# Performance work log

Measured on AMD Instinct MI355X. Metric: run time of the kernel, lower is better.

Reference implementation:

```python
import jax, jax.numpy as jnp
import numpy as np

VOCAB = 32002        # len(tokenizer) + 2
N_HIDDEN = 512
N_COND = 1024
MAX_LENGTH = 15
BATCH = 256


def setup_inputs() -> dict:
    key = jax.random.key(0)
    ks = jax.random.split(key, 12)
    s = 0.02
    return {
        "caption": jax.random.randint(ks[0], (BATCH, 1), 0, VOCAB, dtype=jnp.int64) if jax.config.jax_enable_x64 else jax.random.randint(ks[0], (BATCH, 1), 0, VOCAB, dtype=jnp.int32),
        "img": jax.random.normal(ks[1], (BATCH, N_COND), dtype=jnp.float32),
        "embedding": jax.random.normal(ks[2], (VOCAB, N_HIDDEN), dtype=jnp.float32) * s,
        "W_cond": jax.random.normal(ks[3], (N_HIDDEN, N_COND), dtype=jnp.float32) * s,
        "b_cond": jnp.zeros((N_HIDDEN,), dtype=jnp.float32),
        "w_ih": jax.random.normal(ks[4], (3 * N_HIDDEN, N_HIDDEN), dtype=jnp.float32) * s,
        "w_hh": jax.random.normal(ks[5], (3 * N_HIDDEN, N_HIDDEN), dtype=jnp.float32) * s,
        "b_ih": jnp.zeros((3 * N_HIDDEN,), dtype=jnp.float32),
        "b_hh": jnp.zeros((3 * N_HIDDEN,), dtype=jnp.float32),
        "W_pred": jax.random.normal(ks[6], (VOCAB, N_HIDDEN), dtype=jnp.float32) * s,
        "b_pred": jnp.zeros((VOCAB,), dtype=jnp.float32),
    }


def gru_cell(x, h, w_ih, w_hh, b_ih, b_hh):
    # PyTorch GRUCell math: gates ordered (reset, update, new)
    gi = x @ w_ih.T + b_ih   # [B, 3H]
    gh = h @ w_hh.T + b_hh   # [B, 3H]
    i_r, i_z, i_n = jnp.split(gi, 3, axis=-1)
    h_r, h_z, h_n = jnp.split(gh, 3, axis=-1)
    r = jax.nn.sigmoid(i_r + h_r)
    z = jax.nn.sigmoid(i_z + h_z)
    n = jnp.tanh(i_n + r * h_n)
    return (1.0 - z) * n + z * h


def reference(caption, img, embedding, W_cond, b_cond, w_ih, w_hh, b_ih, b_hh, W_pred, b_pred):
    h0 = img @ W_cond.T + b_cond           # [B, H] initial GRU hidden state
    tok0 = caption[:, 0].astype(jnp.int32)  # seed token

    def step(carry, _):
        h, tok = carry
        x = embedding[tok]                              # [B, H] gather
        h_new = gru_cell(x, h, w_ih, w_hh, b_ih, b_hh)  # [B, H]
        logits = h_new @ W_pred.T + b_pred              # [B, V]
        nxt = jnp.argmax(logits, axis=-1).astype(jnp.int32)  # top-1 == topk(1)
        return (h_new, nxt), nxt

    (_, _), toks = jax.lax.scan(step, (h0, tok0), None, length=MAX_LENGTH - 1)
    # toks: [T-1, B] -> predictions [B, T] with seed token in column 0
    preds = jnp.concatenate([tok0[:, None], toks.T], axis=1)
    return preds
```

## Files before the change

### kernel.cpp

```cpp
#include <hip/hip_runtime.h>
#include <math.h>

#define BATCH 256
#define NH 512
#define NCOND 1024
#define NV 32002
#define NT 15
#define NVT_F32 501
#define NVT_MF  251

#define SP_P  4096256
#define SP_IH 196608
#define SP_HH 196608
#define SP_C  131072
#define SPLIT_W_BLOCKS 16001
#define SPLIT_S_BLOCKS 2048

typedef short short8 __attribute__((ext_vector_type(8)));
typedef float float4v __attribute__((ext_vector_type(4)));

__device__ __forceinline__ void async_load16(const void* g, void* l){
  __builtin_amdgcn_global_load_lds(
      (const __attribute__((address_space(1))) void*)g,
      (__attribute__((address_space(3))) void*)l, 16, 0, 0);
}

__device__ __forceinline__ void split2(float x, unsigned short& hi, unsigned short& lo){
  unsigned u = __float_as_uint(x);
  unsigned r = u + 0x7fffu + ((u >> 16) & 1u);
  hi = (unsigned short)(r >> 16);
  float fh = __uint_as_float(r & 0xffff0000u);
  float res = x - fh;
  unsigned u2 = __float_as_uint(res);
  unsigned r2 = u2 + 0x7fffu + ((u2 >> 16) & 1u);
  lo = (unsigned short)(r2 >> 16);
}

__device__ __forceinline__ unsigned long long pack_key(float v, int idx){
  unsigned u = __float_as_uint(v);
  u = (u & 0x80000000u) ? ~u : (u | 0x80000000u);
  return ((unsigned long long)u << 32) | (unsigned)(0x7fffffff - idx);
}
__device__ __forceinline__ int key_tok(unsigned long long k){
  return 0x7fffffff - (int)(unsigned)(k & 0xffffffffu);
}

__global__ void k_seed(const int* __restrict__ cap, int* __restrict__ preds){
  int b = threadIdx.x;
  preds[b*NT + 0] = cap[b];
}

__global__ __launch_bounds__(256) void k_split_w(const float* __restrict__ Wp,
    unsigned short* __restrict__ Whi, unsigned short* __restrict__ Wlo){
  size_t i = (size_t)blockIdx.x * 256 + threadIdx.x;
  float4 v = *(const float4*)(Wp + i*4);
  unsigned short h0,l0,h1,l1,h2,l2,h3,l3;
  split2(v.x,h0,l0); split2(v.y,h1,l1); split2(v.z,h2,l2); split2(v.w,h3,l3);
  ushort4 hs = {h0,h1,h2,h3};
  ushort4 ls = {l0,l1,l2,l3};
  *(ushort4*)(Whi + i*4) = hs;
  *(ushort4*)(Wlo + i*4) = ls;
}

__global__ __launch_bounds__(256) void k_split_small(
    const float* __restrict__ wih, const float* __restrict__ whh,
    const float* __restrict__ Wc,
    unsigned short* __restrict__ W6hi, unsigned short* __restrict__ W6lo,
    unsigned short* __restrict__ Wchi, unsigned short* __restrict__ Wclo){
  size_t i = (size_t)blockIdx.x * 256 + threadIdx.x;
  const float* src; unsigned short *dh, *dl; size_t off;
  if (i < SP_IH){ src = wih; dh = W6hi; dl = W6lo; off = i; }
  else if (i < SP_IH + SP_HH){
    src = whh; dh = W6hi + 786432; dl = W6lo + 786432; off = i - SP_IH;
  } else { src = Wc; dh = Wchi; dl = Wclo; off = i - SP_IH - SP_HH; }
  float4 v = *(const float4*)(src + off*4);
  unsigned short h0,l0,h1,l1,h2,l2,h3,l3;
  split2(v.x,h0,l0); split2(v.y,h1,l1); split2(v.z,h2,l2); split2(v.w,h3,l3);
  ushort4 hs = {h0,h1,h2,h3};
  ushort4 ls = {l0,l1,l2,l3};
  *(ushort4*)(dh + off*4) = hs;
  *(ushort4*)(dl + off*4) = ls;
}

__global__ __launch_bounds__(256) void k_h0_mf(
    const float* __restrict__ img,
    const unsigned short* __restrict__ Wchi, const unsigned short* __restrict__ Wclo,
    const float* __restrict__ bc,
    float* __restrict__ h0,
    unsigned short* __restrict__ hhi, unsigned short* __restrict__ hlo){
  __shared__ __align__(16) unsigned short sA[2][16*64];
  __shared__ __align__(16) unsigned short sB[2][64*64];
  int tid = threadIdx.x, w = tid >> 6, lane = tid & 63;
  int jbase = blockIdx.x * 16, bbase = blockIdx.y * 64;
  int r16 = lane & 15, q = lane >> 4;
  float4v acc = {0.f,0.f,0.f,0.f};
  for (int k0 = 0; k0 < NCOND; k0 += 64){
    {
      int arr = w >> 1, t = w & 1;
      int a = t*8 + (lane >> 3);
      int p = (lane & 7) ^ (lane >> 3);
      const unsigned short* gs = (arr ? Wclo : Wchi) + (size_t)(jbase + a)*NCOND + k0 + p*8;
      async_load16(gs, (char*)&sA[arr][0] + t*1024);
    }
    #pragma unroll
    for (int i = 0; i < 2; i++){
      int u = tid + 256*i;
      int b = u >> 3, s = u & 7;
      int p = s ^ (b & 7);
      const float* gp = img + (size_t)(bbase + b)*NCOND + k0 + p*8;
      float4 f0 = *(const float4*)gp, f1 = *(const float4*)(gp + 4);
      short8 hv, lv; unsigned short hh, ll;
      split2(f0.x,hh,ll); hv[0]=(short)hh; lv[0]=(short)ll;
      split2(f0.y,hh,ll); hv[1]=(short)hh; lv[1]=(short)ll;
      split2(f0.z,hh,ll); hv[2]=(short)hh; lv[2]=(short)ll;
      split2(f0.w,hh,ll); hv[3]=(short)hh; lv[3]=(short)ll;
      split2(f1.x,hh,ll); hv[4]=(short)hh; lv[4]=(short)ll;
      split2(f1.y,hh,ll); hv[5]=(short)hh; lv[5]=(short)ll;
      split2(f1.z,hh,ll); hv[6]=(short)hh; lv[6]=(short)ll;
      split2(f1.w,hh,ll); hv[7]=(short)hh; lv[7]=(short)ll;
      *(short8*)((char*)&sB[0][0] + b*128 + s*16) = hv;
      *(short8*)((char*)&sB[1][0] + b*128 + s*16) = lv;
    }
    __syncthreads();
    int rb = w*16 + r16;
    #pragma unroll
    for (int kh = 0; kh < 2; kh++){
      int pa = kh*4 + q;
      int offA = r16*128 + ((pa ^ (r16 & 7))*16);
      int offB = rb*128 + ((pa ^ (rb & 7))*16);
      short8 ah = *(const short8*)((const char*)&sA[0][0] + offA);
      short8 al = *(const short8*)((const char*)&sA[1][0] + offA);
      short8 bh = *(const short8*)((const char*)&sB[0][0] + offB);
      short8 bl = *(const short8*)((const char*)&sB[1][0] + offB);
      acc = __builtin_amdgcn_mfma_f32_16x16x32_bf16(ah, bh, acc, 0,0,0);
      acc = __builtin_amdgcn_mfma_f32_16x16x32_bf16(ah, bl, acc, 0,0,0);
      acc = __builtin_amdgcn_mfma_f32_16x16x32_bf16(al, bh, acc, 0,0,0);
    }
    __syncthreads();
  }
  int b = bbase + w*16 + r16;
  #pragma unroll
  for (int reg = 0; reg < 4; reg++){
    int j = jbase + q*4 + reg;
    float val = acc[reg] + bc[j];
    h0[(size_t)b*NH + j] = val;
    unsigned short sh, sl; split2(val, sh, sl);
    hhi[(size_t)b*NH + j] = sh;
    hlo[(size_t)b*NH + j] = sl;
  }
}

__global__ __launch_bounds__(256) void k_gru_mf(
    const int* __restrict__ cap,
    const unsigned long long* __restrict__ slot_prev,
    const float* __restrict__ emb,
    const unsigned short* __restrict__ W6hi, const unsigned short* __restrict__ W6lo,
    const unsigned short* __restrict__ Hhi, const unsigned short* __restrict__ Hlo,
    const float* __restrict__ bih, const float* __restrict__ bhh,
    const float* __restrict__ hprev, float* __restrict__ hnew,
    unsigned short* __restrict__ nhhi, unsigned short* __restrict__ nhlo,
    int* __restrict__ preds, int use_caption, int pred_col){
  __shared__ __align__(16) unsigned short sAh[96*128];
  __shared__ __align__(16) unsigned short sAl[96*128];
  __shared__ __align__(16) unsigned short sXh[32*128];
  __shared__ __align__(16) unsigned short sXl[32*128];
  __shared__ __align__(16) unsigned short sHh[32*128];
  __shared__ __align__(16) unsigned short sHl[32*128];
  __shared__ float comb[2][768];
  __shared__ int tok[32];
  int tid = threadIdx.x, w = tid >> 6, lane = tid & 63;
  int jbase = blockIdx.x * 16, bbase = blockIdx.y * 32;
  int bsub = w & 1, grp = w >> 1;
  int b16 = lane & 15, q = lane >> 4;

  if (tid < 32){
    int t;
    if (use_caption) t = cap[bbase + tid];
    else {
      t = key_tok(slot_prev[bbase + tid]);
      if (blockIdx.x == 0) preds[(bbase + tid)*NT + pred_col] = t;
    }
    tok[tid] = t;
  }
  __syncthreads();
  int tr0 = tok[tid >> 4];
  int tr1 = tok[16 + (tid >> 4)];

  float4v acc[3];
  #pragma unroll
  for (int g = 0; g < 3; g++) acc[g] = (float4v){0.f,0.f,0.f,0.f};

  for (int k0 = 0; k0 < NH; k0 += 128){
    #pragma unroll
    for (int i = 0; i < 12; i++){
      int idx = w*12 + i;
      int arr = idx >= 24, t = arr ? (idx - 24) : idx;
      int row = t*4 + (lane >> 4);
      int glocal = row >> 4, jr = row & 15;
      int slot = (lane & 15) ^ (row & 15);
      const unsigned short* gs = (arr ? W6lo : W6hi)
          + (size_t)(glocal*512 + jbase + jr)*NH + k0 + slot*8;
      async_load16(gs, (char*)(arr ? sAl : sAh) + t*1024);
    }
    #pragma unroll
    for (int i = 0; i < 4; i++){
      int idx = w*4 + i;
      int arr = idx >= 8, t = idx & 7;
      int row = t*4 + (lane >> 4);
      int slot = (lane & 15) ^ (row & 15);
      const unsigned short* gs = (arr ? Hlo : Hhi)
          + (size_t)(bbase + row)*NH + k0 + slot*8;
      async_load16(gs, (char*)(arr ? sHl : sHh) + t*1024);
    }
    #pragma unroll
    for (int i = 0; i < 2; i++){
      int u = tid + 256*i;
      int row = u >> 4, slot = u & 15;
      int phys = slot ^ (row & 15);
      int tr = i ? tr1 : tr0;
      const float* gp = emb + (size_t)tr*NH + k0 + slot*8;
      float4 f0 = *(const float4*)gp, f1 = *(const float4*)(gp + 4);
      short8 hv, lv; unsigned short hh, ll;
      split2(f0.x,hh,ll); hv[0]=(short)hh; lv[0]=(short)ll;
      split2(f0.y,hh,ll); hv[1]=(short)hh; lv[1]=(short)ll;
      split2(f0.z,hh,ll); hv[2]=(short)hh; lv[2]=(short)ll;
      split2(f0.w,hh,ll); hv[3]=(short)hh; lv[3]=(short)ll;
      split2(f1.x,hh,ll); hv[4]=(short)hh; lv[4]=(short)ll;
      split2(f1.y,hh,ll); hv[5]=(short)hh; lv[5]=(short)ll;
      split2(f1.z,hh,ll); hv[6]=(short)hh; lv[6]=(short)ll;
      split2(f1.w,hh,ll); hv[7]=(short)hh; lv[7]=(short)ll;
      *(short8*)((char*)sXh + row*256 + phys*16) = hv;
      *(short8*)((char*)sXl + row*256 + phys*16) = lv;
    }
    __syncthreads();
    #pragma unroll
    for (int kh = 0; kh < 4; kh++){
      int phys = (kh*4 + q) ^ b16;
      int boff = (bsub*16 + b16)*256 + phys*16;
      short8 bh = grp ? *(const short8*)((const char*)sHh + boff)
                      : *(const short8*)((const char*)sXh + boff);
      short8 bl = grp ? *(const short8*)((const char*)sHl + boff)
                      : *(const short8*)((const char*)sXl + boff);
      #pragma unroll
      for (int gi = 0; gi < 3; gi++){
        int row = (grp*3 + gi)*16 + b16;
        int aoff = row*256 + phys*16;
        short8 ah = *(const short8*)((const char*)sAh + aoff);
        short8 al = *(const short8*)((const char*)sAl + aoff);
        acc[gi] = __builtin_amdgcn_mfma_f32_16x16x32_bf16(ah, bh, acc[gi], 0,0,0);
        acc[gi] = __builtin_amdgcn_mfma_f32_16x16x32_bf16(ah, bl, acc[gi], 0,0,0);
        acc[gi] = __builtin_amdgcn_mfma_f32_16x16x32_bf16(al, bh, acc[gi], 0,0,0);
      }
    }
    __syncthreads();
  }

  if (grp == 1){
    #pragma unroll
    for (int gi = 0; gi < 3; gi++)
      #pragma unroll
      for (int reg = 0; reg < 4; reg++)
        comb[bsub][gi*256 + b16*16 + q*4 + reg] = acc[gi][reg];
  }
  __syncthreads();
  if (grp == 0){
    int b = bbase + bsub*16 + b16;
    #pragma unroll
    for (int reg = 0; reg < 4; reg++){
      int jl = q*4 + reg;
      int j = jbase + jl;
      float hr = comb[bsub][0*256 + b16*16 + jl];
      float hz = comb[bsub][1*256 + b16*16 + jl];
      float hn = comb[bsub][2*256 + b16*16 + jl];
      float gr = acc[0][reg] + hr + bih[j] + bhh[j];
      float gz = acc[1][reg] + hz + bih[j+NH] + bhh[j+NH];
      float in_ = acc[2][reg] + bih[j+2*NH];
      float hn_ = hn + bhh[j+2*NH];
      float r = 1.f/(1.f + expf(-gr));
      float z = 1.f/(1.f + expf(-gz));
      float n = tanhf(in_ + r*hn_);
      float hp = hprev[(size_t)b*NH + j];
      float val = (1.f - z)*n + z*hp;
      hnew[(size_t)b*NH + j] = val;
      unsigned short sh, sl; split2(val, sh, sl);
      nhhi[(size_t)b*NH + j] = sh;
      nhlo[(size_t)b*NH + j] = sl;
    }
  }
}

__global__ __launch_bounds__(256) void k_pred_mf(
    const unsigned short* __restrict__ Hhi, const unsigned short* __restrict__ Hlo,
    const unsigned short* __restrict__ Whi, const unsigned short* __restrict__ Wlo,
    const float* __restrict__ bp,
    unsigned long long* __restrict__ slot){
  __shared__ __align__(16) unsigned short sAh[128*64];
  __shared__ __align__(16) unsigned short sAl[128*64];
  __shared__ __align__(16) unsigned short sBh[128*64];
  __shared__ __align__(16) unsigned short sBl[128*64];
  __shared__ float sval[256];
  __shared__ int   sidx[256];
  int tid = threadIdx.x, w = tid >> 6, lane = tid & 63;
  int vt = blockIdx.x, vbase = vt*128, bbase = blockIdx.y*128;
  int mhalf = w & 1, nhalf = w >> 1;
  unsigned short* mybuf = (w==0)?sAh:(w==1)?sAl:(w==2)?sBh:sBl;
  const unsigned short* gsrc = (w==0)?Whi:(w==1)?Wlo:(w==2)?Hhi:Hlo;
  int rowbase = (w < 2) ? vbase : bbase;
  int isA = (w < 2);
  int rl = lane >> 3, sl = lane & 7;
  int pq = sl ^ rl;
  float4v acc[4][4];
  #pragma unroll
  for (int mi=0;mi<4;mi++)
    #pragma unroll
    for (int ni=0;ni<4;ni++) acc[mi][ni] = (float4v){0.f,0.f,0.f,0.f};
  int q = lane >> 4, b16 = lane & 15;

  for (int k0 = 0; k0 < NH; k0 += 64){
    #pragma unroll
    for (int t = 0; t < 16; t++){
      int grow = rowbase + t*8 + rl;
      if (isA && grow > NV-1) grow = NV-1;
      const unsigned short* gp = gsrc + (size_t)grow*NH + k0 + pq*8;
      async_load16(gp, (char*)mybuf + t*1024);
    }
    __syncthreads();
    #pragma unroll
    for (int kh = 0; kh < 2; kh++){
      int pa = kh*4 + q;
      short8 ah[4], al[4], bh[4], bl[4];
      #pragma unroll
      for (int mi=0;mi<4;mi++){
        int r = mhalf*64 + mi*16 + b16;
        int off = r*128 + ((pa ^ (r & 7))*16);
        ah[mi] = *(const short8*)((const char*)sAh + off);
        al[mi] = *(const short8*)((const char*)sAl + off);
      }
      #pragma unroll
      for (int ni=0;ni<4;ni++){
        int r = nhalf*64 + ni*16 + b16;
        int off = r*128 + ((pa ^ (r & 7))*16);
        bh[ni] = *(const short8*)((const char*)sBh + off);
        bl[ni] = *(const short8*)((const char*)sBl + off);
      }
      #pragma unroll
      for (int mi=0;mi<4;mi++)
        #pragma unroll
        for (int ni=0;ni<4;ni++){
          acc[mi][ni] = __builtin_amdgcn_mfma_f32_16x16x32_bf16(ah[mi], bh[ni], acc[mi][ni], 0,0,0);
          acc[mi][ni] = __builtin_amdgcn_mfma_f32_16x16x32_bf16(ah[mi], bl[ni], acc[mi][ni], 0,0,0);
          acc[mi][ni] = __builtin_amdgcn_mfma_f32_16x16x32_bf16(al[mi], bh[ni], acc[mi][ni], 0,0,0);
        }
    }
    __syncthreads();
  }

  float bestv[4] = {-INFINITY,-INFINITY,-INFINITY,-INFINITY};
  int   besti[4] = {0x7fffffff,0x7fffffff,0x7fffffff,0x7fffffff};
  #pragma unroll
  for (int mi=0;mi<4;mi++){
    #pragma unroll
    for (int reg=0;reg<4;reg++){
      int v = vbase + mhalf*64 + mi*16 + q*4 + reg;
      if (v < NV){
        float bpv = bp[v];
        #pragma unroll
        for (int ni=0;ni<4;ni++){
          float cand = acc[mi][ni][reg] + bpv;
          if (cand > bestv[ni] || (cand == bestv[ni] && v < besti[ni])){
            bestv[ni] = cand; besti[ni] = v;
          }
        }
      }
    }
  }
  #pragma unroll
  for (int ni=0;ni<4;ni++){
    #pragma unroll
    for (int off=16; off<=32; off<<=1){
      float ov = __shfl_xor(bestv[ni], off);
      int   oi = __shfl_xor(besti[ni], off);
      if (ov > bestv[ni] || (ov == bestv[ni] && oi < besti[ni])){
        bestv[ni] = ov; besti[ni] = oi;
      }
    }
    if (lane < 16){
      sval[w*64 + ni*16 + b16] = bestv[ni];
      sidx[w*64 + ni*16 + b16] = besti[ni];
    }
  }
  __syncthreads();
  if (tid < 128){
    int nh = tid >> 6;
    int wA = nh*2, wB = nh*2 + 1;
    int slotid = tid & 63;
    float vA = sval[wA*64 + slotid], vB = sval[wB*64 + slotid];
    int   iA = sidx[wA*64 + slotid], iB = sidx[wB*64 + slotid];
    bool takeB = (vB > vA) || (vB == vA && iB < iA);
    float bv = takeB ? vB : vA;
    int   bi = takeB ? iB : iA;
    atomicMax(slot + bbase + tid, pack_key(bv, bi));
  }
}

__global__ void k_fin_slot(const unsigned long long* __restrict__ slot,
                           int* __restrict__ preds){
  int b = threadIdx.x;
  preds[b*NT + (NT-1)] = key_tok(slot[b]);
}

__global__ __launch_bounds__(256) void k_h0_fb(const float* __restrict__ img,
                                            const float* __restrict__ Wc,
                                            const float* __restrict__ bc,
                                            float* __restrict__ h0){
  __shared__ float As[64*36];
  __shared__ float Bs[64*36];
  int tid = threadIdx.x;
  int tx = tid & 15, ty = tid >> 4;
  int jbase = blockIdx.x * 64;
  int bbase = blockIdx.y * 64;
  int lrow = tid >> 3;
  int lc4  = (tid & 7) << 2;
  float acc[4][4] = {};
  for (int k0 = 0; k0 < NCOND; k0 += 32){
    #pragma unroll
    for (int rr = 0; rr < 64; rr += 32){
      *(float4*)&As[(lrow+rr)*36 + lc4] =
          *(const float4*)(img + (size_t)(bbase+lrow+rr)*NCOND + k0 + lc4);
      *(float4*)&Bs[(lrow+rr)*36 + lc4] =
          *(const float4*)(Wc + (size_t)(jbase+lrow+rr)*NCOND + k0 + lc4);
    }
    __syncthreads();
    #pragma unroll
    for (int kk = 0; kk < 32; kk += 4){
      float4 a[4], w[4];
      #pragma unroll
      for (int i=0;i<4;i++) a[i] = *(float4*)&As[(ty+16*i)*36+kk];
      #pragma unroll
      for (int j=0;j<4;j++) w[j] = *(float4*)&Bs[(tx+16*j)*36+kk];
      #pragma unroll
      for (int i=0;i<4;i++)
        #pragma unroll
        for (int j=0;j<4;j++)
          acc[i][j] += a[i].x*w[j].x + a[i].y*w[j].y + a[i].z*w[j].z + a[i].w*w[j].w;
    }
    __syncthreads();
  }
  #pragma unroll
  for (int i=0;i<4;i++){
    int b = bbase + ty + 16*i;
    #pragma unroll
    for (int j=0;j<4;j++){
      int jj = jbase + tx + 16*j;
      h0[(size_t)b*NH + jj] = acc[i][j] + bc[jj];
    }
  }
}

__global__ __launch_bounds__(256) void k_pred_f32(const float* __restrict__ h,
                                              const float* __restrict__ Wp,
                                              const float* __restrict__ bp,
                                              float* __restrict__ pval,
                                              int* __restrict__ pidx){
  __shared__ float As[64*36];
  __shared__ float Bs[64*36];
  __shared__ float rv[64*16];
  __shared__ int   ri[64*16];
  int tid = threadIdx.x;
  int tx = tid & 15, ty = tid >> 4;
  int vt = blockIdx.x;
  int vbase = vt * 64;
  int bbase = blockIdx.y * 64;
  int lrow = tid >> 3;
  int lc4  = (tid & 7) << 2;
  float acc[4][4] = {};
  for (int k0 = 0; k0 < NH; k0 += 32){
    #pragma unroll
    for (int rr = 0; rr < 64; rr += 32){
      *(float4*)&As[(lrow+rr)*36 + lc4] =
          *(const float4*)(h + (size_t)(bbase+lrow+rr)*NH + k0 + lc4);
      int v = vbase + lrow + rr;
      float4 wv = make_float4(0.f,0.f,0.f,0.f);
      if (v < NV) wv = *(const float4*)(Wp + (size_t)v*NH + k0 + lc4);
      *(float4*)&Bs[(lrow+rr)*36 + lc4] = wv;
    }
    __syncthreads();
    #pragma unroll
    for (int kk = 0; kk < 32; kk += 4){
      float4 a[4], wv[4];
      #pragma unroll
      for (int i=0;i<4;i++) a[i] = *(float4*)&As[(ty+16*i)*36+kk];
      #pragma unroll
      for (int j=0;j<4;j++) wv[j] = *(float4*)&Bs[(tx+16*j)*36+kk];
      #pragma unroll
      for (int i=0;i<4;i++)
        #pragma unroll
        for (int j=0;j<4;j++)
          acc[i][j] += a[i].x*wv[j].x + a[i].y*wv[j].y + a[i].z*wv[j].z + a[i].w*wv[j].w;
    }
    __syncthreads();
  }
  #pragma unroll
  for (int i=0;i<4;i++){
    int bl = ty + 16*i;
    float best = -INFINITY; int bidx = 0;
    #pragma unroll
    for (int j=0;j<4;j++){
      int v = vbase + tx + 16*j;
      if (v < NV){
        float val = acc[i][j] + bp[v];
        if (val > best){ best = val; bidx = v; }
      }
    }
    rv[bl*16+tx] = best; ri[bl*16+tx] = bidx;
  }
  __syncthreads();
  if (tid < 64){
    float best = -INFINITY; int bidx = 0;
    #pragma unroll
    for (int t=0;t<16;t++){
      float v = rv[tid*16+t];
      if (v > best){ best = v; bidx = ri[tid*16+t]; }
    }
    pval[vt*BATCH + bbase + tid] = best;
    pidx[vt*BATCH + bbase + tid] = bidx;
  }
}

__global__ __launch_bounds__(256) void k_gru_fb(const int* __restrict__ cap,
    const float* __restrict__ pval, const int* __restrict__ pidx,
    const float* __restrict__ emb,
    const float* __restrict__ wih, const float* __restrict__ whh,
    const float* __restrict__ bih, const float* __restrict__ bhh,
    const float* __restrict__ hprev, float* __restrict__ hnew,
    int* __restrict__ preds, int use_caption, int pred_col, int nvt){
  __shared__ int   s_tok[32];
  __shared__ float rav[32*8];
  __shared__ int   rai[32*8];
  __shared__ float xs[32*36];
  __shared__ float hs[32*36];
  __shared__ float wis[3*16*36];
  __shared__ float whs[3*16*36];
  int tid = threadIdx.x;
  int tx = tid & 15, ty = tid >> 4;
  int jbase = blockIdx.x * 16;
  int bbase = blockIdx.y * 32;

  if (use_caption){
    if (tid < 32) s_tok[tid] = cap[bbase + tid];
  } else {
    int bl = tid >> 3, l8 = tid & 7;
    float best = -INFINITY; int bidx = 0x7fffffff;
    for (int p = l8; p < nvt; p += 8){
      float v = pval[p*BATCH + bbase + bl];
      int   i = pidx[p*BATCH + bbase + bl];
      if (v > best || (v == best && i < bidx)){ best = v; bidx = i; }
    }
    rav[bl*8 + l8] = best; rai[bl*8 + l8] = bidx;
    __syncthreads();
    if (tid < 32){
      float bb = -INFINITY; int bi = 0x7fffffff;
      #pragma unroll
      for (int t=0;t<8;t++){
        float v = rav[tid*8+t]; int i = rai[tid*8+t];
        if (v > bb || (v == bb && i < bi)){ bb = v; bi = i; }
      }
      s_tok[tid] = bi;
      if (blockIdx.x == 0) preds[(bbase+tid)*NT + pred_col] = bi;
    }
  }
  __syncthreads();

  float acc[2][6] = {};
  int lrow = tid >> 3;
  int lc4  = (tid & 7) << 2;
  for (int k0 = 0; k0 < NH; k0 += 32){
    int tokr = s_tok[lrow];
    *(float4*)&xs[lrow*36 + lc4] =
        *(const float4*)(emb + (size_t)tokr*NH + k0 + lc4);
    *(float4*)&hs[lrow*36 + lc4] =
        *(const float4*)(hprev + (size_t)(bbase+lrow)*NH + k0 + lc4);
    #pragma unroll
    for (int qy = tid; qy < 768; qy += 256){
      int g  = qy >> 7;
      int r  = (qy >> 3) & 15;
      int cc = (qy & 7) << 2;
      const float* wsrc = (g < 3) ? wih : whh;
      int gg = (g < 3) ? g : (g - 3);
      float* dst = (g < 3) ? wis : whs;
      *(float4*)&dst[gg*576 + r*36 + cc] =
          *(const float4*)(wsrc + (size_t)(gg*NH + jbase + r)*NH + k0 + cc);
    }
    __syncthreads();
    #pragma unroll
    for (int kk = 0; kk < 32; kk += 4){
      float4 x0 = *(float4*)&xs[ty*36+kk];
      float4 x1 = *(float4*)&xs[(ty+16)*36+kk];
      float4 h0v = *(float4*)&hs[ty*36+kk];
      float4 h1v = *(float4*)&hs[(ty+16)*36+kk];
      #pragma unroll
      for (int g=0; g<3; g++){
        float4 wi4 = *(float4*)&wis[g*576 + tx*36 + kk];
        float4 wh4 = *(float4*)&whs[g*576 + tx*36 + kk];
        acc[0][g]   += x0.x*wi4.x + x0.y*wi4.y + x0.z*wi4.z + x0.w*wi4.w;
        acc[1][g]   += x1.x*wi4.x + x1.y*wi4.y + x1.z*wi4.z + x1.w*wi4.w;
        acc[0][3+g] += h0v.x*wh4.x + h0v.y*wh4.y + h0v.z*wh4.z + h0v.w*wh4.w;
        acc[1][3+g] += h1v.x*wh4.x + h1v.y*wh4.y + h1v.z*wh4.z + h1v.w*wh4.w;
      }
    }
    __syncthreads();
  }
  int j = jbase + tx;
  float bi_r = bih[j], bi_z = bih[j+NH], bi_n = bih[j+2*NH];
  float bh_r = bhh[j], bh_z = bhh[j+NH], bh_n = bhh[j+2*NH];
  #pragma unroll
  for (int i=0;i<2;i++){
    int b = bbase + ty + 16*i;
    float r = 1.f/(1.f + expf(-((acc[i][0]+bi_r) + (acc[i][3]+bh_r))));
    float z = 1.f/(1.f + expf(-((acc[i][1]+bi_z) + (acc[i][4]+bh_z))));
    float n = tanhf((acc[i][2]+bi_n) + r*(acc[i][5]+bh_n));
    float hp = hprev[(size_t)b*NH + j];
    hnew[(size_t)b*NH + j] = (1.f - z)*n + z*hp;
  }
}

__global__ void k_fin(const float* __restrict__ pval, const int* __restrict__ pidx,
                      int* __restrict__ preds, int col, int nvt){
  __shared__ float rav[32*8];
  __shared__ int   rai[32*8];
  int tid = threadIdx.x;
  int bbase = blockIdx.x * 32;
  int bl = tid >> 3, l8 = tid & 7;
  float best = -INFINITY; int bidx = 0x7fffffff;
  for (int p = l8; p < nvt; p += 8){
    float v = pval[p*BATCH + bbase + bl];
    int   i = pidx[p*BATCH + bbase + bl];
    if (v > best || (v == best && i < bidx)){ best = v; bidx = i; }
  }
  rav[bl*8+l8] = best; rai[bl*8+l8] = bidx;
  __syncthreads();
  if (tid < 32){
    float bb = -INFINITY; int bi = 0x7fffffff;
    #pragma unroll
    for (int t=0;t<8;t++){
      float v = rav[tid*8+t]; int i = rai[tid*8+t];
      if (v > bb || (v == bb && i < bi)){ bb = v; bi = i; }
    }
    preds[(bbase+tid)*NT + col] = bi;
  }
}

extern "C" void kernel_launch(void* const* d_in, const int* in_sizes, int n_in,
                              void* d_out, int out_size, void* d_ws, size_t ws_size,
                              hipStream_t stream){
  const int*   cap = (const int*)d_in[0];
  const float* img = (const float*)d_in[1];
  const float* emb = (const float*)d_in[2];
  const float* Wc  = (const float*)d_in[3];
  const float* bc  = (const float*)d_in[4];
  const float* wih = (const float*)d_in[5];
  const float* whh = (const float*)d_in[6];
  const float* bih = (const float*)d_in[7];
  const float* bhh = (const float*)d_in[8];
  const float* Wp  = (const float*)d_in[9];
  const float* bp  = (const float*)d_in[10];
  int* preds = (int*)d_out;

  char* p = (char*)d_ws;
  float* h0b = (float*)p;                   p += (size_t)BATCH*NH*4;
  float* h1b = (float*)p;                   p += (size_t)BATCH*NH*4;
  float* pval = (float*)p;                  p += (size_t)NVT_F32*BATCH*4;
  int*   pidx = (int*)p;                    p += (size_t)NVT_F32*BATCH*4;
  unsigned short* Hhi0 = (unsigned short*)p; p += (size_t)BATCH*NH*2;
  unsigned short* Hlo0 = (unsigned short*)p; p += (size_t)BATCH*NH*2;
  unsigned short* Hhi1 = (unsigned short*)p; p += (size_t)BATCH*NH*2;
  unsigned short* Hlo1 = (unsigned short*)p; p += (size_t)BATCH*NH*2;
  unsigned short* Whi = (unsigned short*)p;  p += (size_t)NV*NH*2;
  unsigned short* Wlo = (unsigned short*)p;  p += (size_t)NV*NH*2;
  unsigned short* W6hi = (unsigned short*)p; p += (size_t)3072*NH*2;
  unsigned short* W6lo = (unsigned short*)p; p += (size_t)3072*NH*2;
  unsigned short* Wchi = (unsigned short*)p; p += (size_t)NH*NCOND*2;
  unsigned short* Wclo = (unsigned short*)p; p += (size_t)NH*NCOND*2;
  unsigned long long* slots = (unsigned long long*)p; p += (size_t)NT*BATCH*8;
  size_t need = (size_t)(p - (char*)d_ws);

  bool use_mfma = (ws_size >= need);

  k_seed<<<1, 256, 0, stream>>>(cap, preds);
  float* hb[2] = {h0b, h1b};

  if (use_mfma){
    hipMemsetAsync(slots, 0, (size_t)NT*BATCH*8, stream);
    k_split_small<<<dim3(SPLIT_S_BLOCKS), 256, 0, stream>>>(wih, whh, Wc,
                                                            W6hi, W6lo, Wchi, Wclo);
    k_h0_mf<<<dim3(NH/16, BATCH/64), 256, 0, stream>>>(img, Wchi, Wclo, bc,
                                                       h0b, Hhi0, Hlo0);
    unsigned short* Hhs[2] = {Hhi0, Hhi1};
    unsigned short* Hls[2] = {Hlo0, Hlo1};
    k_gru_mf<<<dim3(NH/16, BATCH/32), 256, 0, stream>>>(cap, slots, emb,
        W6hi, W6lo, Hhs[0], Hls[0], bih, bhh,
        hb[0], hb[1], Hhs[1], Hls[1], preds, 1, 0);
    k_split_w<<<dim3(SPLIT_W_BLOCKS), 256, 0, stream>>>(Wp, Whi, Wlo);
    k_pred_mf<<<dim3(NVT_MF, 2), 256, 0, stream>>>(Hhs[1], Hls[1], Whi, Wlo,
                                                   bp, slots + 1*BATCH);
    for (int s = 2; s <= NT-1; s++){
      int pi = (s-1)&1, ci = s&1;
      k_gru_mf<<<dim3(NH/16, BATCH/32), 256, 0, stream>>>(cap, slots + (size_t)(s-1)*BATCH,
          emb, W6hi, W6lo, Hhs[pi], Hls[pi], bih, bhh,
          hb[pi], hb[ci], Hhs[ci], Hls[ci], preds, 0, s-1);
      k_pred_mf<<<dim3(NVT_MF, 2), 256, 0, stream>>>(Hhs[ci], Hls[ci], Whi, Wlo,
                                                     bp, slots + (size_t)s*BATCH);
    }
    k_fin_slot<<<1, 256, 0, stream>>>(slots + (size_t)(NT-1)*BATCH, preds);
  } else {
    k_h0_fb<<<dim3(NH/64, BATCH/64), 256, 0, stream>>>(img, Wc, bc, h0b);
    for (int s = 1; s <= NT-1; s++){
      const float* hprev = hb[(s-1)&1];
      float* hnew = hb[s&1];
      k_gru_fb<<<dim3(NH/16, BATCH/32), 256, 0, stream>>>(cap, pval, pidx, emb, wih, whh,
                                                       bih, bhh, hprev, hnew,
                                                       preds, (s==1)?1:0, s-1, NVT_F32);
      k_pred_f32<<<dim3(NVT_F32, BATCH/64), 256, 0, stream>>>(hnew, Wp, bp, pval, pidx);
    }
    k_fin<<<dim3(BATCH/32), 256, 0, stream>>>(pval, pidx, preds, NT-1, NVT_F32);
  }
}
```

Baseline: 836.6 us.

## Use single bf16 logits pass with error-bounded candidate rescoring in fp32

Replaces the three-MFMA split-bf16 prediction GEMM with a single bf16 hi*hi MFMA pass that writes all logits and a per-row approximate max. A new scan kernel uses an error bound built from the max W row norm and the per-batch hidden norm to select candidate tokens, then recomputes their logits exactly in double precision to pick the argmax. This removes two thirds of the MFMA work and the Wlo buffer traffic. In exchange it writes and rereads a full V×B logit matrix every step, and correctness depends on the heuristic SCAN_C bound being large enough.

```diff
diff --git a/kernel.cpp b/kernel.cpp
--- a/kernel.cpp
+++ b/kernel.cpp
@@ -9,12 +9,14 @@
 #define NVT_F32 501
 #define NVT_MF  251
 
-#define SP_P  4096256
 #define SP_IH 196608
 #define SP_HH 196608
 #define SP_C  131072
 #define SPLIT_W_BLOCKS 16001
 #define SPLIT_S_BLOCKS 2048
+
+#define SCAN_C 0.011f
+#define MAXCAND 1024
 
 typedef short short8 __attribute__((ext_vector_type(8)));
 typedef float float4v __attribute__((ext_vector_type(4)));
@@ -36,6 +38,12 @@
   lo = (unsigned short)(r2 >> 16);
 }
 
+__device__ __forceinline__ unsigned short bf16rn(float x){
+  unsigned u = __float_as_uint(x);
+  unsigned r = u + 0x7fffu + ((u >> 16) & 1u);
+  return (unsigned short)(r >> 16);
+}
+
 __device__ __forceinline__ unsigned long long pack_key(float v, int idx){
   unsigned u = __float_as_uint(v);
   u = (u & 0x80000000u) ? ~u : (u | 0x80000000u);
@@ -44,6 +52,11 @@
 __device__ __forceinline__ int key_tok(unsigned long long k){
   return 0x7fffffff - (int)(unsigned)(k & 0xffffffffu);
 }
+__device__ __forceinline__ float key_val(unsigned long long k){
+  unsigned u = (unsigned)(k >> 32);
+  u = (u & 0x80000000u) ? (u ^ 0x80000000u) : ~u;
+  return __uint_as_float(u);
+}
 
 __global__ void k_seed(const int* __restrict__ cap, int* __restrict__ preds){
   int b = threadIdx.x;
@@ -51,15 +64,21 @@
 }
 
 __global__ __launch_bounds__(256) void k_split_w(const float* __restrict__ Wp,
-    unsigned short* __restrict__ Whi, unsigned short* __restrict__ Wlo){
-  size_t i = (size_t)blockIdx.x * 256 + threadIdx.x;
+    unsigned short* __restrict__ Whi, float* __restrict__ wn2){
+  __shared__ float rs[2];
+  int tid = threadIdx.x;
+  size_t i = (size_t)blockIdx.x * 256 + tid;
   float4 v = *(const float4*)(Wp + i*4);
-  unsigned short h0,l0,h1,l1,h2,l2,h3,l3;
-  split2(v.x,h0,l0); split2(v.y,h1,l1); split2(v.z,h2,l2); split2(v.w,h3,l3);
-  ushort4 hs = {h0,h1,h2,h3};
-  ushort4 ls = {l0,l1,l2,l3};
+  ushort4 hs = {bf16rn(v.x), bf16rn(v.y), bf16rn(v.z), bf16rn(v.w)};
   *(ushort4*)(Whi + i*4) = hs;
-  *(ushort4*)(Wlo + i*4) = ls;
+  float ss = v.x*v.x + v.y*v.y + v.z*v.z + v.w*v.w;
+  #pragma unroll
+  for (int off = 1; off < 64; off <<= 1) ss += __shfl_xor(ss, off);
+  if (tid < 2) rs[tid] = 0.f;
+  __syncthreads();
+  if ((tid & 63) == 0) atomicAdd(&rs[tid >> 7], ss);
+  __syncthreads();
+  if (tid < 2) atomicMax((int*)wn2, __float_as_int(rs[tid]));
 }
 
 __global__ __launch_bounds__(256) void k_split_small(
@@ -159,7 +178,8 @@
     const float* __restrict__ bih, const float* __restrict__ bhh,
     const float* __restrict__ hprev, float* __restrict__ hnew,
     unsigned short* __restrict__ nhhi, unsigned short* __restrict__ nhlo,
-    int* __restrict__ preds, int use_caption, int pred_col){
+    int* __restrict__ preds, float* __restrict__ hsq,
+    int use_caption, int pred_col){
   __shared__ __align__(16) unsigned short sAh[96*128];
   __shared__ __align__(16) unsigned short sAl[96*128];
   __shared__ __align__(16) unsigned short sXh[32*128];
@@ -265,6 +285,7 @@
   __syncthreads();
   if (grp == 0){
     int b = bbase + bsub*16 + b16;
+    float ssq = 0.f;
     #pragma unroll
     for (int reg = 0; reg < 4; reg++){
       int jl = q*4 + reg;
@@ -285,72 +306,68 @@
       unsigned short sh, sl; split2(val, sh, sl);
       nhhi[(size_t)b*NH + j] = sh;
       nhlo[(size_t)b*NH + j] = sl;
-    }
-  }
-}
-
-__global__ __launch_bounds__(256) void k_pred_mf(
-    const unsigned short* __restrict__ Hhi, const unsigned short* __restrict__ Hlo,
-    const unsigned short* __restrict__ Whi, const unsigned short* __restrict__ Wlo,
+      ssq += val*val;
+    }
+    ssq += __shfl_xor(ssq, 16);
+    ssq += __shfl_xor(ssq, 32);
+    if (q == 0) atomicAdd(hsq + b, ssq);
+  }
+}
+
+__global__ __launch_bounds__(256) void k_pred1(
+    const unsigned short* __restrict__ Hhi,
+    const unsigned short* __restrict__ Whi,
     const float* __restrict__ bp,
-    unsigned long long* __restrict__ slot){
-  __shared__ __align__(16) unsigned short sAh[128*64];
-  __shared__ __align__(16) unsigned short sAl[128*64];
-  __shared__ __align__(16) unsigned short sBh[128*64];
-  __shared__ __align__(16) unsigned short sBl[128*64];
+    float* __restrict__ Lg,
+    unsigned long long* __restrict__ mslot){
+  __shared__ __align__(16) unsigned short sA[128*64];
+  __shared__ __align__(16) unsigned short sB[128*64];
   __shared__ float sval[256];
   __shared__ int   sidx[256];
   int tid = threadIdx.x, w = tid >> 6, lane = tid & 63;
-  int vt = blockIdx.x, vbase = vt*128, bbase = blockIdx.y*128;
+  int vbase = blockIdx.x*128, bbase = blockIdx.y*128;
   int mhalf = w & 1, nhalf = w >> 1;
-  unsigned short* mybuf = (w==0)?sAh:(w==1)?sAl:(w==2)?sBh:sBl;
-  const unsigned short* gsrc = (w==0)?Whi:(w==1)?Wlo:(w==2)?Hhi:Hlo;
-  int rowbase = (w < 2) ? vbase : bbase;
-  int isA = (w < 2);
-  int rl = lane >> 3, sl = lane & 7;
-  int pq = sl ^ rl;
+  int isA = (w < 2) ? 1 : 0;
+  const unsigned short* gsrc = isA ? Whi : Hhi;
+  unsigned short* dbuf = isA ? sA : sB;
+  int rowb = isA ? vbase : bbase;
+  int th0 = (w & 1) * 8;
+  int rl = lane >> 3, sl = lane & 7, pq = sl ^ rl;
+  int q = lane >> 4, b16 = lane & 15;
   float4v acc[4][4];
   #pragma unroll
   for (int mi=0;mi<4;mi++)
     #pragma unroll
     for (int ni=0;ni<4;ni++) acc[mi][ni] = (float4v){0.f,0.f,0.f,0.f};
-  int q = lane >> 4, b16 = lane & 15;
 
   for (int k0 = 0; k0 < NH; k0 += 64){
     #pragma unroll
-    for (int t = 0; t < 16; t++){
-      int grow = rowbase + t*8 + rl;
+    for (int t = 0; t < 8; t++){
+      int tt = th0 + t;
+      int grow = rowb + tt*8 + rl;
       if (isA && grow > NV-1) grow = NV-1;
-      const unsigned short* gp = gsrc + (size_t)grow*NH + k0 + pq*8;
-      async_load16(gp, (char*)mybuf + t*1024);
+      async_load16(gsrc + (size_t)grow*NH + k0 + pq*8, (char*)dbuf + tt*1024);
     }
     __syncthreads();
     #pragma unroll
     for (int kh = 0; kh < 2; kh++){
       int pa = kh*4 + q;
-      short8 ah[4], al[4], bh[4], bl[4];
+      short8 a8[4], b8[4];
       #pragma unroll
       for (int mi=0;mi<4;mi++){
         int r = mhalf*64 + mi*16 + b16;
-        int off = r*128 + ((pa ^ (r & 7))*16);
-        ah[mi] = *(const short8*)((const char*)sAh + off);
-        al[mi] = *(const short8*)((const char*)sAl + off);
+        a8[mi] = *(const short8*)((const char*)sA + r*128 + ((pa ^ (r & 7))*16));
       }
       #pragma unroll
       for (int ni=0;ni<4;ni++){
         int r = nhalf*64 + ni*16 + b16;
-        int off = r*128 + ((pa ^ (r & 7))*16);
-        bh[ni] = *(const short8*)((const char*)sBh + off);
-        bl[ni] = *(const short8*)((const char*)sBl + off);
+        b8[ni] = *(const short8*)((const char*)sB + r*128 + ((pa ^ (r & 7))*16));
       }
       #pragma unroll
       for (int mi=0;mi<4;mi++)
         #pragma unroll
-        for (int ni=0;ni<4;ni++){
-          acc[mi][ni] = __builtin_amdgcn_mfma_f32_16x16x32_bf16(ah[mi], bh[ni], acc[mi][ni], 0,0,0);
-          acc[mi][ni] = __builtin_amdgcn_mfma_f32_16x16x32_bf16(ah[mi], bl[ni], acc[mi][ni], 0,0,0);
-          acc[mi][ni] = __builtin_amdgcn_mfma_f32_16x16x32_bf16(al[mi], bh[ni], acc[mi][ni], 0,0,0);
-        }
+        for (int ni=0;ni<4;ni++)
+          acc[mi][ni] = __builtin_amdgcn_mfma_f32_16x16x32_bf16(a8[mi], b8[ni], acc[mi][ni], 0,0,0);
     }
     __syncthreads();
   }
@@ -367,6 +384,7 @@
         #pragma unroll
         for (int ni=0;ni<4;ni++){
           float cand = acc[mi][ni][reg] + bpv;
+          Lg[(size_t)v*BATCH + bbase + nhalf*64 + ni*16 + b16] = cand;
           if (cand > bestv[ni] || (cand == bestv[ni] && v < besti[ni])){
             bestv[ni] = cand; besti[ni] = v;
           }
@@ -399,7 +417,87 @@
     bool takeB = (vB > vA) || (vB == vA && iB < iA);
     float bv = takeB ? vB : vA;
     int   bi = takeB ? iB : iA;
-    atomicMax(slot + bbase + tid, pack_key(bv, bi));
+    atomicMax(mslot + bbase + tid, pack_key(bv, bi));
+  }
+}
+
+__device__ __forceinline__ void wave_exact_dot(int v, int b, int lane,
+    const float* __restrict__ Wp, const float* __restrict__ h,
+    const float* __restrict__ bp, unsigned long long* __restrict__ slot){
+  const float* wr = Wp + (size_t)v*NH + lane*8;
+  const float* hr = h  + (size_t)b*NH + lane*8;
+  float4 w0 = *(const float4*)wr, w1 = *(const float4*)(wr + 4);
+  float4 h0 = *(const float4*)hr, h1 = *(const float4*)(hr + 4);
+  double s = (double)w0.x*h0.x + (double)w0.y*h0.y
+           + (double)w0.z*h0.z + (double)w0.w*h0.w
+           + (double)w1.x*h1.x + (double)w1.y*h1.y
+           + (double)w1.z*h1.z + (double)w1.w*h1.w;
+  #pragma unroll
+  for (int off = 1; off < 64; off <<= 1) s += __shfl_xor(s, off);
+  if (lane == 0) atomicMax(slot + b, pack_key((float)(s + (double)bp[v]), v));
+}
+
+__global__ __launch_bounds__(256) void k_scan(
+    const float* __restrict__ Lg,
+    const unsigned long long* __restrict__ mslot,
+    const float* __restrict__ hsq,
+    const float* __restrict__ wn2,
+    const float* __restrict__ h,
+    const float* __restrict__ Wp,
+    const float* __restrict__ bp,
+    unsigned long long* __restrict__ slot){
+  __shared__ float thr[256];
+  __shared__ int cl[MAXCAND];
+  __shared__ int cnt;
+  __shared__ int over;
+  int tid = threadIdx.x, w = tid >> 6, lane = tid & 63;
+  int vbase = blockIdx.x * 128;
+  if (tid == 0){ cnt = 0; over = 0; }
+  {
+    float wn = sqrtf(wn2[0]);
+    float M = key_val(mslot[tid]);
+    float B = SCAN_C * wn * sqrtf(hsq[tid]);
+    thr[tid] = M - 2.f*B;
+  }
+  __syncthreads();
+  #pragma unroll 4
+  for (int it = 0; it < 32; it++){
+    int v = vbase + it*4 + (tid >> 6);
+    if (v < NV){
+      int b0 = (tid & 63)*4;
+      float4 vv = *(const float4*)(Lg + (size_t)v*BATCH + b0);
+      #pragma unroll
+      for (int e = 0; e < 4; e++){
+        float val = (e==0)?vv.x:(e==1)?vv.y:(e==2)?vv.z:vv.w;
+        if (val >= thr[b0 + e]){
+          int id = atomicAdd(&cnt, 1);
+          if (id < MAXCAND) cl[id] = v*BATCH + (b0 + e);
+          else over = 1;
+        }
+      }
+    }
+  }
+  __syncthreads();
+  int n = cnt < MAXCAND ? cnt : MAXCAND;
+  for (int c = w; c < n; c += 4){
+    int pk = cl[c];
+    wave_exact_dot(pk >> 8, pk & 255, lane, Wp, h, bp, slot);
+  }
+  if (over){
+    for (int r = w; r < 128; r += 4){
+      int v = vbase + r;
+      if (v < NV){
+        for (int bc = 0; bc < 4; bc++){
+          int b = bc*64 + lane;
+          float val = Lg[(size_t)v*BATCH + b];
+          unsigned long long m = __ballot(val >= thr[b]);
+          while (m){
+            int bl = __ffsll((unsigned long long)m) - 1; m &= m - 1;
+            wave_exact_dot(v, bc*64 + bl, lane, Wp, h, bp, slot);
+          }
+        }
+      }
+    }
   }
 }
 
@@ -676,12 +774,16 @@
   unsigned short* Hhi1 = (unsigned short*)p; p += (size_t)BATCH*NH*2;
   unsigned short* Hlo1 = (unsigned short*)p; p += (size_t)BATCH*NH*2;
   unsigned short* Whi = (unsigned short*)p;  p += (size_t)NV*NH*2;
-  unsigned short* Wlo = (unsigned short*)p;  p += (size_t)NV*NH*2;
   unsigned short* W6hi = (unsigned short*)p; p += (size_t)3072*NH*2;
   unsigned short* W6lo = (unsigned short*)p; p += (size_t)3072*NH*2;
   unsigned short* Wchi = (unsigned short*)p; p += (size_t)NH*NCOND*2;
   unsigned short* Wclo = (unsigned short*)p; p += (size_t)NH*NCOND*2;
+  float* Lg = (float*)p;                     p += (size_t)NV*BATCH*4;
   unsigned long long* slots = (unsigned long long*)p; p += (size_t)NT*BATCH*8;
+  unsigned long long* mslots = (unsigned long long*)p; p += (size_t)NT*BATCH*8;
+  float* hsqb = (float*)p;                   p += (size_t)NT*BATCH*4;
+  float* wn2 = (float*)p;                    p += 16;
+  size_t zero_bytes = (size_t)NT*BATCH*8*2 + (size_t)NT*BATCH*4 + 16;
   size_t need = (size_t)(p - (char*)d_ws);
 
   bool use_mfma = (ws_size >= need);
@@ -690,7 +792,7 @@
   float* hb[2] = {h0b, h1b};
 
   if (use_mfma){
-    hipMemsetAsync(slots, 0, (size_t)NT*BATCH*8, stream);
+    hipMemsetAsync(slots, 0, zero_bytes, stream);
     k_split_small<<<dim3(SPLIT_S_BLOCKS), 256, 0, stream>>>(wih, whh, Wc,
                                                             W6hi, W6lo, Wchi, Wclo);
     k_h0_mf<<<dim3(NH/16, BATCH/64), 256, 0, stream>>>(img, Wchi, Wclo, bc,
@@ -699,17 +801,21 @@
     unsigned short* Hls[2] = {Hlo0, Hlo1};
     k_gru_mf<<<dim3(NH/16, BATCH/32), 256, 0, stream>>>(cap, slots, emb,
         W6hi, W6lo, Hhs[0], Hls[0], bih, bhh,
-        hb[0], hb[1], Hhs[1], Hls[1], preds, 1, 0);
-    k_split_w<<<dim3(SPLIT_W_BLOCKS), 256, 0, stream>>>(Wp, Whi, Wlo);
-    k_pred_mf<<<dim3(NVT_MF, 2), 256, 0, stream>>>(Hhs[1], Hls[1], Whi, Wlo,
-                                                   bp, slots + 1*BATCH);
+        hb[0], hb[1], Hhs[1], Hls[1], preds, hsqb + 1*BATCH, 1, 0);
+    k_split_w<<<dim3(SPLIT_W_BLOCKS), 256, 0, stream>>>(Wp, Whi, wn2);
+    k_pred1<<<dim3(NVT_MF, 2), 256, 0, stream>>>(Hhs[1], Whi, bp, Lg,
+                                                 mslots + 1*BATCH);
+    k_scan<<<dim3(NVT_MF), 256, 0, stream>>>(Lg, mslots + 1*BATCH,
+        hsqb + 1*BATCH, wn2, hb[1], Wp, bp, slots + 1*BATCH);
     for (int s = 2; s <= NT-1; s++){
       int pi = (s-1)&1, ci = s&1;
       k_gru_mf<<<dim3(NH/16, BATCH/32), 256, 0, stream>>>(cap, slots + (size_t)(s-1)*BATCH,
           emb, W6hi, W6lo, Hhs[pi], Hls[pi], bih, bhh,
-          hb[pi], hb[ci], Hhs[ci], Hls[ci], preds, 0, s-1);
-      k_pred_mf<<<dim3(NVT_MF, 2), 256, 0, stream>>>(Hhs[ci], Hls[ci], Whi, Wlo,
-                                                     bp, slots + (size_t)s*BATCH);
+          hb[pi], hb[ci], Hhs[ci], Hls[ci], preds, hsqb + (size_t)s*BATCH, 0, s-1);
+      k_pred1<<<dim3(NVT_MF, 2), 256, 0, stream>>>(Hhs[ci], Whi, bp, Lg,
+                                                   mslots + (size_t)s*BATCH);
+      k_scan<<<dim3(NVT_MF), 256, 0, stream>>>(Lg, mslots + (size_t)s*BATCH,
+          hsqb + (size_t)s*BATCH, wn2, hb[ci], Wp, bp, slots + (size_t)s*BATCH);
     }
     k_fin_slot<<<1, 256, 0, stream>>>(slots + (size_t)(NT-1)*BATCH, preds);
   } else {
```

Measured after the change: 1.163 ms. +39.0%, slower.
